# Optimization experiments

Hardware: AMD Instinct MI355X
Metric: run time of the kernel (lower is better)

## Reference

```python
import jax, jax.numpy as jnp
import numpy as np

N_NODES = 50000


def setup_inputs() -> dict:
    key = jax.random.key(0)
    ks = jax.random.split(key, 9)
    B, N, E, IN = 4, N_NODES, 800000, 32
    x = jax.random.normal(ks[0], (B, N, IN), dtype=jnp.float32)
    edge_index = jax.random.randint(ks[1], (2, E), 0, N, dtype=jnp.int64)
    edge_attr = jax.random.normal(ks[2], (E, 1), dtype=jnp.float32)
    W1 = jax.random.normal(ks[3], (2 * IN + 1, 32), dtype=jnp.float32) * 0.1
    b1 = jax.random.normal(ks[4], (32,), dtype=jnp.float32) * 0.1
    W2 = jax.random.normal(ks[5], (32, 30), dtype=jnp.float32) * 0.1
    b2 = jax.random.normal(ks[6], (30,), dtype=jnp.float32) * 0.1
    W3 = jax.random.normal(ks[7], (30, 32), dtype=jnp.float32) * 0.1
    b3 = jax.random.normal(ks[8], (32,), dtype=jnp.float32) * 0.1
    return {"x": x, "edge_index": edge_index, "edge_attr": edge_attr,
            "W1": W1, "b1": b1, "W2": W2, "b2": b2, "W3": W3, "b3": b3}


def reference(x, edge_index, edge_attr, W1, b1, W2, b2, W3, b3):
    B, N, _ = x.shape
    src, tgt = edge_index[0], edge_index[1]
    # normalize edge attributes over edges (torch .std uses ddof=1)
    ea = (edge_attr - edge_attr.mean(axis=0)) / edge_attr.std(axis=0, ddof=1)
    node_src = x[:, src]      # [B, E, in]
    node_tgt = x[:, tgt]      # [B, E, in]
    ea_b = jnp.broadcast_to(ea[None], (B,) + ea.shape)
    h = jnp.concatenate([node_src, node_tgt, ea_b], axis=-1)  # [B, E, 2*in+1]
    h = jax.nn.sigmoid(h @ W1 + b1)
    h = jax.nn.sigmoid(h @ W2 + b2)   # [B, E, 30]
    seg = lambda vals, idx: jax.ops.segment_sum(vals, idx, num_segments=N)
    out_add = jax.vmap(seg, in_axes=(0, None))(h, tgt)    # [B, N, 30]
    out_sub = jax.vmap(seg, in_axes=(0, None))(-h, src)   # [B, N, 30]
    out = out_add + out_sub
    return jax.nn.sigmoid(out @ W3 + b3)  # [B, N, out_dim]
```

## Files before the change

### kernel.cpp

```cpp
#include <hip/hip_runtime.h>
#include <math.h>

#define B_SZ 4
#define IN_F 32
#define H1_F 32
#define H2_F 30
#define TPW 16
#define HREP 16

typedef unsigned int uint;
typedef unsigned short ushort;
typedef __attribute__((ext_vector_type(8))) short bf16x8;
typedef __attribute__((ext_vector_type(4))) float f32x4;

__device__ __forceinline__ float fastrcp(float x) {
#if __has_builtin(__builtin_amdgcn_rcpf)
    return __builtin_amdgcn_rcpf(x);
#else
    return 1.f / x;
#endif
}
__device__ __forceinline__ float sigmoidf_(float x) {
    return fastrcp(1.f + __expf(-x));
}

__device__ __forceinline__ ushort f2bf(float f) {
    uint u = __float_as_uint(f);
    return (ushort)((u + 0x7FFFu + ((u >> 16) & 1u)) >> 16);
}
__device__ __forceinline__ float bf2f(ushort v) { return __uint_as_float(((uint)v) << 16); }
__device__ __forceinline__ uint pk2(float a, float b) {
    return (uint)f2bf(a) | ((uint)f2bf(b) << 16);
}

union Frag { bf16x8 v; ushort us[8]; uint u[4]; };

__global__ void __launch_bounds__(256) stats_hist_kernel(
    const float* __restrict__ ea, const int* __restrict__ ei,
    float2* __restrict__ psums, int* __restrict__ cnt, int E, int N) {
    int e = blockIdx.x * 256 + threadIdx.x;
    int* myc = cnt + (size_t)(blockIdx.x & (HREP - 1)) * N;
    float a = (e < E) ? ea[e] : 0.f;
    if (e < E) {
        atomicAdd(&myc[ei[E + e]], 1);
        atomicAdd(&myc[ei[e]], 1);
    }
    float v = a, v2 = a * a;
    for (int off = 32; off > 0; off >>= 1) {
        v  += __shfl_down(v, off);
        v2 += __shfl_down(v2, off);
    }
    __shared__ float s1[4], s2[4];
    int wid = threadIdx.x >> 6, lane = threadIdx.x & 63;
    if (lane == 0) { s1[wid] = v; s2[wid] = v2; }
    __syncthreads();
    if (threadIdx.x == 0) {
        float2 p;
        p.x = s1[0] + s1[1] + s1[2] + s1[3];
        p.y = s2[0] + s2[1] + s2[2] + s2[3];
        psums[blockIdx.x] = p;
    }
}

__global__ void __launch_bounds__(256) sums_reduce_kernel(
    const float2* __restrict__ psums, float* __restrict__ sums, int nblk) {
    float v = 0.f, v2 = 0.f;
    for (int i = threadIdx.x; i < nblk; i += 256) {
        float2 p = psums[i];
        v += p.x; v2 += p.y;
    }
    for (int off = 32; off > 0; off >>= 1) {
        v  += __shfl_down(v, off);
        v2 += __shfl_down(v2, off);
    }
    __shared__ float s1[4], s2[4];
    int wid = threadIdx.x >> 6, lane = threadIdx.x & 63;
    if (lane == 0) { s1[wid] = v; s2[wid] = v2; }
    __syncthreads();
    if (threadIdx.x == 0) {
        sums[0] = s1[0] + s1[1] + s1[2] + s1[3];
        sums[1] = s2[0] + s2[1] + s2[2] + s2[3];
    }
}

__global__ void __launch_bounds__(256) xcvt_kernel(const float* __restrict__ x,
                                                   ushort* __restrict__ xb,
                                                   long long n8) {
    long long i = (long long)blockIdx.x * 256 + threadIdx.x;
    if (i >= n8) return;
    const float4* p = (const float4*)(x + i * 8);
    float4 v0 = p[0], v1 = p[1];
    uint4 o;
    o.x = pk2(v0.x, v0.y); o.y = pk2(v0.z, v0.w);
    o.z = pk2(v1.x, v1.y); o.w = pk2(v1.z, v1.w);
    *(uint4*)(xb + i * 8) = o;
}

__global__ void __launch_bounds__(256) scan1_kernel(const int* __restrict__ cnt,
                                                    int* __restrict__ offs,
                                                    int* __restrict__ bsum, int n) {
    __shared__ int wtot[4];
    int base = blockIdx.x * 1024 + threadIdx.x * 4;
    int4 v = {0, 0, 0, 0};
    if (base + 3 < n) {
#pragma unroll
        for (int r = 0; r < HREP; r++) {
            int4 t = *(const int4*)(cnt + (size_t)r * n + base);
            v.x += t.x; v.y += t.y; v.z += t.z; v.w += t.w;
        }
    } else {
        for (int r = 0; r < HREP; r++) {
            const int* c = cnt + (size_t)r * n;
            if (base < n)     v.x += c[base];
            if (base + 1 < n) v.y += c[base + 1];
            if (base + 2 < n) v.z += c[base + 2];
            if (base + 3 < n) v.w += c[base + 3];
        }
    }
    int s = v.x + v.y + v.z + v.w;
    int incl = s;
    int lane = threadIdx.x & 63;
    for (int d = 1; d < 64; d <<= 1) {
        int t = __shfl_up(incl, d);
        if (lane >= d) incl += t;
    }
    int wid = threadIdx.x >> 6;
    if (lane == 63) wtot[wid] = incl;
    __syncthreads();
    int woff = 0, tot = 0;
#pragma unroll
    for (int w = 0; w < 4; w++) {
        int t = wtot[w];
        if (w < wid) woff += t;
        tot += t;
    }
    int excl = woff + incl - s;
    int4 o;
    o.x = excl; o.y = excl + v.x; o.z = o.y + v.y; o.w = o.z + v.z;
    if (base + 3 < n) *(int4*)(offs + base) = o;
    else {
        if (base < n)     offs[base] = o.x;
        if (base + 1 < n) offs[base + 1] = o.y;
        if (base + 2 < n) offs[base + 2] = o.z;
        if (base + 3 < n) offs[base + 3] = o.w;
    }
    if (threadIdx.x == 0) bsum[blockIdx.x] = tot;
}

__global__ void scan2_kernel(int* __restrict__ bsum, int* __restrict__ offs,
                             int nb, int n) {
    int lane = threadIdx.x;
    if (nb <= 64) {
        int v = (lane < nb) ? bsum[lane] : 0;
        int incl = v;
        for (int d = 1; d < 64; d <<= 1) {
            int t = __shfl_up(incl, d);
            if (lane >= d) incl += t;
        }
        if (lane < nb) bsum[lane] = incl - v;
        if (lane == 63) offs[n] = incl;
    } else if (lane == 0) {
        int run = 0;
        for (int i = 0; i < nb; i++) { int t = bsum[i]; bsum[i] = run; run += t; }
        offs[n] = run;
    }
}

__global__ void __launch_bounds__(256) scan3_kernel(int* __restrict__ offs,
                                                    int* __restrict__ cursor,
                                                    const int* __restrict__ bsum, int n) {
    int base = blockIdx.x * 1024 + threadIdx.x * 4;
    int add = bsum[blockIdx.x];
    if (base + 3 < n) {
        int4 v = *(const int4*)(offs + base);
        v.x += add; v.y += add; v.z += add; v.w += add;
        *(int4*)(offs + base) = v;
        *(int4*)(cursor + base) = v;
    } else {
        for (int k = 0; k < 4; k++) {
            int i = base + k;
            if (i < n) { int v = offs[i] + add; offs[i] = v; cursor[i] = v; }
        }
    }
}

__global__ void __launch_bounds__(256) restore_cursor_kernel(
    const int* __restrict__ offs, int* __restrict__ cursor, int n) {
    int i = blockIdx.x * 256 + threadIdx.x;
    if (i < n) cursor[i] = offs[i];
}

__global__ void __launch_bounds__(256) edge_mlp_slot(
    const ushort* __restrict__ xb,
    const int* __restrict__ ei, const float* __restrict__ ea,
    const float* __restrict__ W1, const float* __restrict__ b1,
    const float* __restrict__ W2, const float* __restrict__ b2,
    const float* __restrict__ sums, int* __restrict__ cursor,
    ushort* __restrict__ h, int E, int N, int tiles, int boff) {
    __shared__ ushort __attribute__((aligned(16))) hbuf[4][16 * 40];
    int w = threadIdx.x >> 6;
    int lane = threadIdx.x & 63;
    int n16 = lane & 15;
    int q = lane >> 4;

    Frag w1f[2][2];
#pragma unroll
    for (int t = 0; t < 2; t++)
#pragma unroll
        for (int s = 0; s < 2; s++)
#pragma unroll
            for (int j = 0; j < 4; j++) {
                int k0 = 32 * s + q * 8 + 2 * j;
                w1f[t][s].u[j] = pk2(W1[(size_t)k0 * 32 + 16 * t + n16],
                                     W1[(size_t)(k0 + 1) * 32 + 16 * t + n16]);
            }
    Frag w2f[2];
#pragma unroll
    for (int t = 0; t < 2; t++) {
        int m = 16 * t + n16;
#pragma unroll
        for (int j = 0; j < 4; j++) {
            int k0 = q * 8 + 2 * j;
            float a = (m < H2_F) ? W2[(size_t)k0 * H2_F + m] : 0.f;
            float d = (m < H2_F) ? W2[(size_t)(k0 + 1) * H2_F + m] : 0.f;
            w2f[t].u[j] = pk2(a, d);
        }
    }
    float b1q[2][4], w1Lq[2][4], b2q[2][4];
#pragma unroll
    for (int t = 0; t < 2; t++)
#pragma unroll
        for (int r = 0; r < 4; r++) {
            int col = 16 * t + q * 4 + r;
            b1q[t][r]  = b1[col];
            w1Lq[t][r] = W1[(size_t)64 * 32 + col];
            b2q[t][r]  = (col < H2_F) ? b2[col] : 0.f;
        }

    float mean = sums[0] / (float)E;
    float var = (sums[1] - (float)E * mean * mean) / (float)(E - 1);
    float istd = rsqrtf(var);

    int el = n16 >> 1;
    int bl = n16 & 1;
    int b  = bl + boff;
    int gw = blockIdx.x * 4 + w;
    int tile0 = gw * TPW;
    if (tile0 >= tiles) return;

    int src, tgt; float eav; bool vrow; Frag a0, a1; int slotraw;
    {
        int eA = tile0 * 8 + el; vrow = eA < E; int c = vrow ? eA : E - 1;
        src = ei[c]; tgt = ei[E + c]; eav = (ea[c] - mean) * istd;
        *(uint4*)&a0.u[0] = *(const uint4*)(xb + ((size_t)b * N + src) * IN_F + q * 8);
        *(uint4*)&a1.u[0] = *(const uint4*)(xb + ((size_t)b * N + tgt) * IN_F + q * 8);
        slotraw = 0;
        if (lane < 16 && vrow)
            slotraw = atomicAdd(&cursor[(lane & 1) ? src : tgt], 1);
    }

    for (int tix = 0; tix < TPW; ++tix) {
        int tile = tile0 + tix;
        if (tile >= tiles) break;

        int nsrc = 0, ntgt = 0; float neav = 0.f; bool nvrow = false; int nslot = 0;
        Frag na0, na1;
        na0.u[0] = na0.u[1] = na0.u[2] = na0.u[3] = 0; na1 = na0;
        bool hn = (tix + 1 < TPW) && (tile + 1 < tiles);
        if (hn) {
            int eA = (tile + 1) * 8 + el; nvrow = eA < E; int c = nvrow ? eA : E - 1;
            nsrc = ei[c]; ntgt = ei[E + c]; neav = (ea[c] - mean) * istd;
            *(uint4*)&na0.u[0] = *(const uint4*)(xb + ((size_t)b * N + nsrc) * IN_F + q * 8);
            *(uint4*)&na1.u[0] = *(const uint4*)(xb + ((size_t)b * N + ntgt) * IN_F + q * 8);
            if (lane < 16 && nvrow)
                nslot = atomicAdd(&cursor[(lane & 1) ? nsrc : ntgt], 1);
        }

        f32x4 acc0, acc1;
#pragma unroll
        for (int r = 0; r < 4; r++) {
            acc0[r] = b1q[0][r] + eav * w1Lq[0][r];
            acc1[r] = b1q[1][r] + eav * w1Lq[1][r];
        }
        acc0 = __builtin_amdgcn_mfma_f32_16x16x32_bf16(w1f[0][0].v, a0.v, acc0, 0, 0, 0);
        acc0 = __builtin_amdgcn_mfma_f32_16x16x32_bf16(w1f[0][1].v, a1.v, acc0, 0, 0, 0);
        acc1 = __builtin_amdgcn_mfma_f32_16x16x32_bf16(w1f[1][0].v, a0.v, acc1, 0, 0, 0);
        acc1 = __builtin_amdgcn_mfma_f32_16x16x32_bf16(w1f[1][1].v, a1.v, acc1, 0, 0, 0);

        uint u0 = pk2(sigmoidf_(acc0[0]), sigmoidf_(acc0[1]));
        uint u1 = pk2(sigmoidf_(acc0[2]), sigmoidf_(acc0[3]));
        uint u2 = pk2(sigmoidf_(acc1[0]), sigmoidf_(acc1[1]));
        uint u3 = pk2(sigmoidf_(acc1[2]), sigmoidf_(acc1[3]));
        uint2 p01 = {u0, u1}, p23 = {u2, u3};
        *(uint2*)&hbuf[w][n16 * 40 + q * 4]      = p01;
        *(uint2*)&hbuf[w][n16 * 40 + 16 + q * 4] = p23;

        Frag ha;
        *(uint4*)&ha.u[0] = *(const uint4*)&hbuf[w][n16 * 40 + q * 8];

        f32x4 c0, c1;
#pragma unroll
        for (int r = 0; r < 4; r++) { c0[r] = b2q[0][r]; c1[r] = b2q[1][r]; }
        c0 = __builtin_amdgcn_mfma_f32_16x16x32_bf16(w2f[0].v, ha.v, c0, 0, 0, 0);
        c1 = __builtin_amdgcn_mfma_f32_16x16x32_bf16(w2f[1].v, ha.v, c1, 0, 0, 0);

        uint g0 = pk2(sigmoidf_(c0[0]), sigmoidf_(c0[1]));
        uint g1 = pk2(sigmoidf_(c0[2]), sigmoidf_(c0[3]));
        uint g2 = pk2(sigmoidf_(c1[0]), sigmoidf_(c1[1]));
        uint g3 = pk2(sigmoidf_(c1[2]), sigmoidf_(c1[3]));

        int slot_t = __shfl(slotraw, el * 2);
        int slot_s = __shfl(slotraw, el * 2 + 1);
        if (vrow) {
            uint* bt = (uint*)(h + (size_t)slot_t * 64 + bl * 32);
            uint2 t01; t01.x = g0; t01.y = g1;
            uint2 t23; t23.x = g2; t23.y = g3;
            *(uint2*)(bt + q * 2)     = t01;
            *(uint2*)(bt + 8 + q * 2) = t23;
            const uint SM = 0x80008000u;
            uint* bs = (uint*)(h + (size_t)slot_s * 64 + bl * 32);
            uint2 s01; s01.x = g0 ^ SM; s01.y = g1 ^ SM;
            uint2 s23; s23.x = g2 ^ SM; s23.y = g3 ^ SM;
            *(uint2*)(bs + q * 2)     = s01;
            *(uint2*)(bs + 8 + q * 2) = s23;
        }

        src = nsrc; tgt = ntgt; eav = neav; vrow = nvrow;
        a0 = na0; a1 = na1; slotraw = nslot;
    }
}

__global__ void __launch_bounds__(256) gather_slot(
    const ushort* __restrict__ h, const int* __restrict__ offs,
    const float* __restrict__ W3, const float* __restrict__ b3,
    float* __restrict__ out, int N, int boff) {
    __shared__ float sW3[H2_F * 32];
    __shared__ float sb3[32];
    __shared__ float sacc[4][2][H2_F];
    for (int i = threadIdx.x; i < H2_F * 32; i += 256) sW3[i] = W3[i];
    if (threadIdx.x < 32) sb3[threadIdx.x] = b3[threadIdx.x];
    __syncthreads();

    int w = threadIdx.x >> 6, lane = threadIdx.x & 63;
    int n = blockIdx.x * 4 + w;
    if (n >= N) return;

    int s = offs[n], e = offs[n + 1];
    int cnt = e - s;
    int sl = (lane >= 30) ? 1 : 0;
    int r = lane - sl * 30;
    if (lane >= 60) r = 0;
    int bl = r / 15, jp = r % 15;
    const uint* p = (const uint*)h + (size_t)(s + sl) * 32 + bl * 16 + jp;
    float a0 = 0.f, a1 = 0.f;
    int i = (lane < 60) ? sl : cnt;
    for (; i + 6 < cnt; i += 8) {
        uint d0 = p[0], d1 = p[64], d2 = p[128], d3 = p[192];
        p += 256;
        a0 += bf2f((ushort)d0) + bf2f((ushort)d1)
            + bf2f((ushort)d2) + bf2f((ushort)d3);
        a1 += bf2f((ushort)(d0 >> 16)) + bf2f((ushort)(d1 >> 16))
            + bf2f((ushort)(d2 >> 16)) + bf2f((ushort)(d3 >> 16));
    }
    for (; i < cnt; i += 2) {
        uint d = p[0];
        p += 64;
        a0 += bf2f((ushort)d);
        a1 += bf2f((ushort)(d >> 16));
    }
    float f0 = __shfl(a0, lane + 30);
    float f1 = __shfl(a1, lane + 30);
    if (lane < 30) {
        sacc[w][bl][jp * 2]     = a0 + f0;
        sacc[w][bl][jp * 2 + 1] = a1 + f1;
    }
    int bl2 = lane >> 5, k = lane & 31;
    float o = sb3[k];
#pragma unroll
    for (int j = 0; j < H2_F; j++) o += sacc[w][bl2][j] * sW3[j * 32 + k];
    out[((size_t)(boff + bl2) * N + n) * 32 + k] = sigmoidf_(o);
}

__global__ void __launch_bounds__(256) scatter_kernel(const int* __restrict__ ei,
                                                      int* __restrict__ cursor,
                                                      int* __restrict__ list, int E, int N) {
    int e = blockIdx.x * 256 + threadIdx.x;
    if (e < E) {
        int tgt = ei[E + e];
        int p = atomicAdd(&cursor[tgt], 1);
        list[p] = e;
        int src = ei[e];
        int q = atomicAdd(&cursor[src], 1);
        list[q] = e | (int)0x80000000u;
    }
}

template<bool USE_XB>
__global__ void __launch_bounds__(256) edge_mlp_mfma2(
    const float* __restrict__ x, const ushort* __restrict__ xb,
    const int* __restrict__ ei, const float* __restrict__ ea,
    const float* __restrict__ W1, const float* __restrict__ b1,
    const float* __restrict__ W2, const float* __restrict__ b2,
    const float* __restrict__ sums, ushort* __restrict__ h,
    int E, int N, int tiles) {
    __shared__ ushort __attribute__((aligned(16))) hbuf[4][16 * 40];
    int w = threadIdx.x >> 6;
    int lane = threadIdx.x & 63;
    int n16 = lane & 15;
    int q = lane >> 4;

    Frag w1f[2][2];
#pragma unroll
    for (int t = 0; t < 2; t++)
#pragma unroll
        for (int s = 0; s < 2; s++)
#pragma unroll
            for (int j = 0; j < 4; j++) {
                int k0 = 32 * s + q * 8 + 2 * j;
                w1f[t][s].u[j] = pk2(W1[(size_t)k0 * 32 + 16 * t + n16],
                                     W1[(size_t)(k0 + 1) * 32 + 16 * t + n16]);
            }
    Frag w2f[2];
#pragma unroll
    for (int t = 0; t < 2; t++) {
        int m = 16 * t + n16;
#pragma unroll
        for (int j = 0; j < 4; j++) {
            int k0 = q * 8 + 2 * j;
            float a = (m < H2_F) ? W2[(size_t)k0 * H2_F + m] : 0.f;
            float d = (m < H2_F) ? W2[(size_t)(k0 + 1) * H2_F + m] : 0.f;
            w2f[t].u[j] = pk2(a, d);
        }
    }
    float b1q[2][4], w1Lq[2][4], b2q[2][4];
#pragma unroll
    for (int t = 0; t < 2; t++)
#pragma unroll
        for (int r = 0; r < 4; r++) {
            int col = 16 * t + q * 4 + r;
            b1q[t][r]  = b1[col];
            w1Lq[t][r] = W1[(size_t)64 * 32 + col];
            b2q[t][r]  = (col < H2_F) ? b2[col] : 0.f;
        }

    float mean = sums[0] / (float)E;
    float var = (sums[1] - (float)E * mean * mean) / (float)(E - 1);
    float istd = rsqrtf(var);

    int b = n16 & 3;
    int eoff = n16 >> 2;
    int gw = blockIdx.x * 4 + w;

    for (int tix = 0; tix < TPW; ++tix) {
        int tile = gw * TPW + tix;
        if (tile >= tiles) break;
        int e0 = tile * 4;
        int eA = e0 + eoff;
        bool vrow = eA < E;
        int eAc = vrow ? eA : E - 1;
        int src = ei[eAc], tgt = ei[E + eAc];
        float eav = (ea[eAc] - mean) * istd;

        Frag a0, a1;
        if (USE_XB) {
            *(uint4*)&a0.u[0] = *(const uint4*)(xb + ((size_t)b * N + src) * IN_F + q * 8);
            *(uint4*)&a1.u[0] = *(const uint4*)(xb + ((size_t)b * N + tgt) * IN_F + q * 8);
        } else {
            const float4* ps = (const float4*)(x + ((size_t)b * N + src) * IN_F + q * 8);
            float4 s0 = ps[0], s1 = ps[1];
            const float4* pt = (const float4*)(x + ((size_t)b * N + tgt) * IN_F + q * 8);
            float4 t0 = pt[0], t1 = pt[1];
            a0.u[0] = pk2(s0.x, s0.y); a0.u[1] = pk2(s0.z, s0.w);
            a0.u[2] = pk2(s1.x, s1.y); a0.u[3] = pk2(s1.z, s1.w);
            a1.u[0] = pk2(t0.x, t0.y); a1.u[1] = pk2(t0.z, t0.w);
            a1.u[2] = pk2(t1.x, t1.y); a1.u[3] = pk2(t1.z, t1.w);
        }

        f32x4 acc0, acc1;
#pragma unroll
        for (int r = 0; r < 4; r++) {
            acc0[r] = b1q[0][r] + eav * w1Lq[0][r];
            acc1[r] = b1q[1][r] + eav * w1Lq[1][r];
        }
        acc0 = __builtin_amdgcn_mfma_f32_16x16x32_bf16(w1f[0][0].v, a0.v, acc0, 0, 0, 0);
        acc0 = __builtin_amdgcn_mfma_f32_16x16x32_bf16(w1f[0][1].v, a1.v, acc0, 0, 0, 0);
        acc1 = __builtin_amdgcn_mfma_f32_16x16x32_bf16(w1f[1][0].v, a0.v, acc1, 0, 0, 0);
        acc1 = __builtin_amdgcn_mfma_f32_16x16x32_bf16(w1f[1][1].v, a1.v, acc1, 0, 0, 0);

        uint u0 = pk2(sigmoidf_(acc0[0]), sigmoidf_(acc0[1]));
        uint u1 = pk2(sigmoidf_(acc0[2]), sigmoidf_(acc0[3]));
        uint u2 = pk2(sigmoidf_(acc1[0]), sigmoidf_(acc1[1]));
        uint u3 = pk2(sigmoidf_(acc1[2]), sigmoidf_(acc1[3]));
        uint2 p01 = {u0, u1}, p23 = {u2, u3};
        *(uint2*)&hbuf[w][n16 * 40 + q * 4]      = p01;
        *(uint2*)&hbuf[w][n16 * 40 + 16 + q * 4] = p23;

        Frag ha;
        *(uint4*)&ha.u[0] = *(const uint4*)&hbuf[w][n16 * 40 + q * 8];

        f32x4 c0, c1;
#pragma unroll
        for (int r = 0; r < 4; r++) { c0[r] = b2q[0][r]; c1[r] = b2q[1][r]; }
        c0 = __builtin_amdgcn_mfma_f32_16x16x32_bf16(w2f[0].v, ha.v, c0, 0, 0, 0);
        c1 = __builtin_amdgcn_mfma_f32_16x16x32_bf16(w2f[1].v, ha.v, c1, 0, 0, 0);

        uint g0 = pk2(sigmoidf_(c0[0]), sigmoidf_(c0[1]));
        uint g1 = pk2(sigmoidf_(c0[2]), sigmoidf_(c0[3]));
        uint g2 = pk2(sigmoidf_(c1[0]), sigmoidf_(c1[1]));
        uint g3 = pk2(sigmoidf_(c1[2]), sigmoidf_(c1[3]));
        if (vrow) {
            uint* base = (uint*)(h + (size_t)(e0 * 4 + n16) * H2_F);
            base[q * 2]     = g0;
            base[q * 2 + 1] = g1;
            base[8 + q * 2] = g2;
            if (q < 3) base[8 + q * 2 + 1] = g3;
        }
    }
}

__global__ void __launch_bounds__(256) gather_final(
    const ushort* __restrict__ h, const int* __restrict__ list,
    const int* __restrict__ offs, const float* __restrict__ W3,
    const float* __restrict__ b3, float* __restrict__ out, int N) {
    __shared__ float sW3[H2_F * 32];
    __shared__ float sb3[32];
    __shared__ float sacc[4][B_SZ][H2_F];
    for (int i = threadIdx.x; i < H2_F * 32; i += 256) sW3[i] = W3[i];
    if (threadIdx.x < 32) sb3[threadIdx.x] = b3[threadIdx.x];
    __syncthreads();

    int w = threadIdx.x >> 6, lane = threadIdx.x & 63;
    int n = blockIdx.x * 4 + w;
    if (n >= N) return;

    if (lane < 60) {
        int bq = lane / 15, jp = lane % 15;
        float a0 = 0.f, a1 = 0.f;
        int s = offs[n], e = offs[n + 1];
        int i = s;
        for (; i + 4 <= e; i += 4) {
            int v0 = list[i], v1 = list[i + 1], v2 = list[i + 2], v3 = list[i + 3];
            uint d0 = *(const uint*)(h + (size_t)(v0 & 0x7FFFFFFF) * 120 + bq * 30 + jp * 2);
            uint d1 = *(const uint*)(h + (size_t)(v1 & 0x7FFFFFFF) * 120 + bq * 30 + jp * 2);
            uint d2 = *(const uint*)(h + (size_t)(v2 & 0x7FFFFFFF) * 120 + bq * 30 + jp * 2);
            uint d3 = *(const uint*)(h + (size_t)(v3 & 0x7FFFFFFF) * 120 + bq * 30 + jp * 2);
            float g0 = (v0 < 0) ? -1.f : 1.f;
            float g1 = (v1 < 0) ? -1.f : 1.f;
            float g2 = (v2 < 0) ? -1.f : 1.f;
            float g3 = (v3 < 0) ? -1.f : 1.f;
            a0 += g0 * bf2f((ushort)d0) + g1 * bf2f((ushort)d1)
                + g2 * bf2f((ushort)d2) + g3 * bf2f((ushort)d3);
            a1 += g0 * bf2f((ushort)(d0 >> 16)) + g1 * bf2f((ushort)(d1 >> 16))
                + g2 * bf2f((ushort)(d2 >> 16)) + g3 * bf2f((ushort)(d3 >> 16));
        }
        for (; i < e; i++) {
            int v = list[i];
            uint d = *(const uint*)(h + (size_t)(v & 0x7FFFFFFF) * 120 + bq * 30 + jp * 2);
            float g = (v < 0) ? -1.f : 1.f;
            a0 += g * bf2f((ushort)d);
            a1 += g * bf2f((ushort)(d >> 16));
        }
        sacc[w][bq][jp * 2]     = a0;
        sacc[w][bq][jp * 2 + 1] = a1;
    }
    int b = lane >> 4, k = lane & 15;
    float o0 = sb3[k], o1 = sb3[k + 16];
#pragma unroll
    for (int j = 0; j < H2_F; j++) {
        float v = sacc[w][b][j];
        o0 += v * sW3[j * 32 + k];
        o1 += v * sW3[j * 32 + k + 16];
    }
    float* op = out + ((size_t)b * N + n) * 32;
    op[k]      = sigmoidf_(o0);
    op[k + 16] = sigmoidf_(o1);
}

extern "C" void kernel_launch(void* const* d_in, const int* in_sizes, int n_in,
                              void* d_out, int out_size, void* d_ws, size_t ws_size,
                              hipStream_t stream) {
    const float* x  = (const float*)d_in[0];
    const int*   ei = (const int*)d_in[1];
    const float* ea = (const float*)d_in[2];
    const float* W1 = (const float*)d_in[3];
    const float* b1 = (const float*)d_in[4];
    const float* W2 = (const float*)d_in[5];
    const float* b2 = (const float*)d_in[6];
    const float* W3 = (const float*)d_in[7];
    const float* b3 = (const float*)d_in[8];
    float* out = (float*)d_out;

    const int E  = in_sizes[2];
    const int N  = in_sizes[0] / (B_SZ * IN_F);
    const int BN = B_SZ * N;
    const int nb = (N + 1023) / 1024;
    const int nblk_stats = (E + 255) / 256;

    char* base = (char*)d_ws;

    size_t off = 0;
    int* cnt    = (int*)(base + off); off += (size_t)HREP * N * 4;
    float* sums = (float*)(base + off); off += 8;
    int* offs   = (int*)(base + off); off += (size_t)(N + 1) * 4;
    int* cursor = (int*)(base + off); off += (size_t)N * 4;
    int* bsum   = (int*)(base + off); off += 4096;
    off = (off + 255) & ~(size_t)255;
    float2* psums = (float2*)(base + off); off += (size_t)nblk_stats * 8;
    off = (off + 255) & ~(size_t)255;
    ushort* h   = (ushort*)(base + off); off += (size_t)2 * E * 128;
    off = (off + 255) & ~(size_t)255;
    ushort* xb  = (ushort*)(base + off); off += (size_t)BN * IN_F * 2;
    size_t needNew = off;

    size_t offB = 0;
    int* cntB    = (int*)(base + offB); offB += (size_t)HREP * N * 4;
    float* sumsB = (float*)(base + offB); offB += 8;
    int* offsB   = (int*)(base + offB); offB += (size_t)(N + 1) * 4;
    int* cursorB = (int*)(base + offB); offB += (size_t)N * 4;
    int* bsumB   = (int*)(base + offB); offB += 4096;
    offB = (offB + 255) & ~(size_t)255;
    float2* psumsB = (float2*)(base + offB); offB += (size_t)nblk_stats * 8;
    int* list    = (int*)(base + offB); offB += (size_t)2 * E * 4;
    offB = (offB + 255) & ~(size_t)255;
    ushort* hB   = (ushort*)(base + offB); offB += (size_t)E * 240;
    offB = (offB + 255) & ~(size_t)255;
    ushort* xbB  = (ushort*)(base + offB);
    size_t needB = offB + (size_t)BN * IN_F * 2;

    if (ws_size >= needNew) {
        const int tiles = (E + 7) / 8;
        const int waves = (tiles + TPW - 1) / TPW;
        const int eblocks = (waves + 3) / 4;
        hipMemsetAsync(cnt, 0, (size_t)HREP * N * 4 + 8, stream);
        stats_hist_kernel<<<nblk_stats, 256, 0, stream>>>(ea, ei, psums, cnt, E, N);
        sums_reduce_kernel<<<1, 256, 0, stream>>>(psums, sums, nblk_stats);
        long long n8 = (long long)BN * IN_F / 8;
        xcvt_kernel<<<(int)((n8 + 255) / 256), 256, 0, stream>>>(x, xb, n8);
        scan1_kernel<<<nb, 256, 0, stream>>>(cnt, offs, bsum, N);
        scan2_kernel<<<1, 64, 0, stream>>>(bsum, offs, nb, N);
        scan3_kernel<<<nb, 256, 0, stream>>>(offs, cursor, bsum, N);
        edge_mlp_slot<<<eblocks, 256, 0, stream>>>(xb, ei, ea, W1, b1, W2, b2,
                                                   sums, cursor, h, E, N, tiles, 0);
        gather_slot<<<(N + 3) / 4, 256, 0, stream>>>(h, offs, W3, b3, out, N, 0);
        restore_cursor_kernel<<<(N + 255) / 256, 256, 0, stream>>>(offs, cursor, N);
        edge_mlp_slot<<<eblocks, 256, 0, stream>>>(xb, ei, ea, W1, b1, W2, b2,
                                                   sums, cursor, h, E, N, tiles, 2);
        gather_slot<<<(N + 3) / 4, 256, 0, stream>>>(h, offs, W3, b3, out, N, 2);
    } else {
        const int tiles = (E + 3) / 4;
        const int waves = (tiles + TPW - 1) / TPW;
        const int eblocks = (waves + 3) / 4;
        bool use_xb = (ws_size >= needB);
        hipMemsetAsync(cntB, 0, (size_t)HREP * N * 4 + 8, stream);
        stats_hist_kernel<<<nblk_stats, 256, 0, stream>>>(ea, ei, psumsB, cntB, E, N);
        sums_reduce_kernel<<<1, 256, 0, stream>>>(psumsB, sumsB, nblk_stats);
        if (use_xb) {
            long long n8 = (long long)BN * IN_F / 8;
            xcvt_kernel<<<(int)((n8 + 255) / 256), 256, 0, stream>>>(x, xbB, n8);
        }
        scan1_kernel<<<nb, 256, 0, stream>>>(cntB, offsB, bsumB, N);
        scan2_kernel<<<1, 64, 0, stream>>>(bsumB, offsB, nb, N);
        scan3_kernel<<<nb, 256, 0, stream>>>(offsB, cursorB, bsumB, N);
        scatter_kernel<<<(E + 255) / 256, 256, 0, stream>>>(ei, cursorB, list, E, N);
        if (use_xb)
            edge_mlp_mfma2<true><<<eblocks, 256, 0, stream>>>(x, xbB, ei, ea, W1, b1,
                                                              W2, b2, sumsB, hB, E, N, tiles);
        else
            edge_mlp_mfma2<false><<<eblocks, 256, 0, stream>>>(x, xbB, ei, ea, W1, b1,
                                                               W2, b2, sumsB, hB, E, N, tiles);
        gather_final<<<(N + 3) / 4, 256, 0, stream>>>(hB, list, offsB, W3, b3, out, N);
    }
}
```

Before: 454.7 us.

## Compute all four batches per edge once and gather via sorted edge list

The edge MLP now processes all four batch elements per edge in one pass, writing h once per edge in edge order instead of twice (signed copies) into per-node slots across two batch-half passes. It builds a CSR list of edge ids tagged with a sign bit via atomics inside the MLP kernel, and the gather reads h indirectly through that list, applying the sign. The xcvt kernel is fused into the stats/histogram kernel, and the restore_cursor kernel is removed. This halves h writes and the number of MLP/gather launches, at the cost of random indirect reads in the gather instead of contiguous slot reads.

```diff
diff --git a/kernel.cpp b/kernel.cpp
--- a/kernel.cpp
+++ b/kernel.cpp
@@ -35,9 +35,20 @@
 
 union Frag { bf16x8 v; ushort us[8]; uint u[4]; };
 
-__global__ void __launch_bounds__(256) stats_hist_kernel(
+__global__ void __launch_bounds__(256) stats_xcvt_kernel(
     const float* __restrict__ ea, const int* __restrict__ ei,
-    float2* __restrict__ psums, int* __restrict__ cnt, int E, int N) {
+    const float* __restrict__ x, float2* __restrict__ psums,
+    int* __restrict__ cnt, ushort* __restrict__ xb,
+    int E, int N, long long n8) {
+    long long i = (long long)blockIdx.x * 256 + threadIdx.x;
+    if (i < n8) {
+        const float4* p = (const float4*)(x + i * 8);
+        float4 v0 = p[0], v1 = p[1];
+        uint4 o;
+        o.x = pk2(v0.x, v0.y); o.y = pk2(v0.z, v0.w);
+        o.z = pk2(v1.x, v1.y); o.w = pk2(v1.z, v1.w);
+        *(uint4*)(xb + i * 8) = o;
+    }
     int e = blockIdx.x * 256 + threadIdx.x;
     int* myc = cnt + (size_t)(blockIdx.x & (HREP - 1)) * N;
     float a = (e < E) ? ea[e] : 0.f;
@@ -81,19 +92,6 @@
         sums[0] = s1[0] + s1[1] + s1[2] + s1[3];
         sums[1] = s2[0] + s2[1] + s2[2] + s2[3];
     }
-}
-
-__global__ void __launch_bounds__(256) xcvt_kernel(const float* __restrict__ x,
-                                                   ushort* __restrict__ xb,
-                                                   long long n8) {
-    long long i = (long long)blockIdx.x * 256 + threadIdx.x;
-    if (i >= n8) return;
-    const float4* p = (const float4*)(x + i * 8);
-    float4 v0 = p[0], v1 = p[1];
-    uint4 o;
-    o.x = pk2(v0.x, v0.y); o.y = pk2(v0.z, v0.w);
-    o.z = pk2(v1.x, v1.y); o.w = pk2(v1.z, v1.w);
-    *(uint4*)(xb + i * 8) = o;
 }
 
 __global__ void __launch_bounds__(256) scan1_kernel(const int* __restrict__ cnt,
@@ -184,19 +182,14 @@
     }
 }
 
-__global__ void __launch_bounds__(256) restore_cursor_kernel(
-    const int* __restrict__ offs, int* __restrict__ cursor, int n) {
-    int i = blockIdx.x * 256 + threadIdx.x;
-    if (i < n) cursor[i] = offs[i];
-}
-
-__global__ void __launch_bounds__(256) edge_mlp_slot(
+__global__ void __launch_bounds__(256) edge_mlp_e4(
     const ushort* __restrict__ xb,
     const int* __restrict__ ei, const float* __restrict__ ea,
     const float* __restrict__ W1, const float* __restrict__ b1,
     const float* __restrict__ W2, const float* __restrict__ b2,
     const float* __restrict__ sums, int* __restrict__ cursor,
-    ushort* __restrict__ h, int E, int N, int tiles, int boff) {
+    int* __restrict__ list, ushort* __restrict__ h,
+    int E, int N, int tiles) {
     __shared__ ushort __attribute__((aligned(16))) hbuf[4][16 * 40];
     int w = threadIdx.x >> 6;
     int lane = threadIdx.x & 63;
@@ -241,39 +234,49 @@
     float var = (sums[1] - (float)E * mean * mean) / (float)(E - 1);
     float istd = rsqrtf(var);
 
-    int el = n16 >> 1;
-    int bl = n16 & 1;
-    int b  = bl + boff;
+    int b  = n16 & 3;
+    int el = n16 >> 2;
     int gw = blockIdx.x * 4 + w;
     int tile0 = gw * TPW;
     if (tile0 >= tiles) return;
 
-    int src, tgt; float eav; bool vrow; Frag a0, a1; int slotraw;
+    int src, tgt; float eav; bool vrow; Frag a0, a1;
     {
-        int eA = tile0 * 8 + el; vrow = eA < E; int c = vrow ? eA : E - 1;
+        int eA = tile0 * 4 + el; vrow = eA < E; int c = vrow ? eA : E - 1;
         src = ei[c]; tgt = ei[E + c]; eav = (ea[c] - mean) * istd;
         *(uint4*)&a0.u[0] = *(const uint4*)(xb + ((size_t)b * N + src) * IN_F + q * 8);
         *(uint4*)&a1.u[0] = *(const uint4*)(xb + ((size_t)b * N + tgt) * IN_F + q * 8);
-        slotraw = 0;
-        if (lane < 16 && vrow)
-            slotraw = atomicAdd(&cursor[(lane & 1) ? src : tgt], 1);
+        if (lane < 8) {
+            int eS = tile0 * 4 + (lane >> 1);
+            if (eS < E) {
+                int node = (lane & 1) ? ei[eS] : ei[E + eS];
+                int s = atomicAdd(&cursor[node], 1);
+                list[s] = eS | (int)(((uint)(lane & 1)) << 31);
+            }
+        }
     }
 
     for (int tix = 0; tix < TPW; ++tix) {
         int tile = tile0 + tix;
         if (tile >= tiles) break;
 
-        int nsrc = 0, ntgt = 0; float neav = 0.f; bool nvrow = false; int nslot = 0;
+        int nsrc = 0, ntgt = 0; float neav = 0.f; bool nvrow = false;
         Frag na0, na1;
         na0.u[0] = na0.u[1] = na0.u[2] = na0.u[3] = 0; na1 = na0;
         bool hn = (tix + 1 < TPW) && (tile + 1 < tiles);
         if (hn) {
-            int eA = (tile + 1) * 8 + el; nvrow = eA < E; int c = nvrow ? eA : E - 1;
+            int eA = (tile + 1) * 4 + el; nvrow = eA < E; int c = nvrow ? eA : E - 1;
             nsrc = ei[c]; ntgt = ei[E + c]; neav = (ea[c] - mean) * istd;
             *(uint4*)&na0.u[0] = *(const uint4*)(xb + ((size_t)b * N + nsrc) * IN_F + q * 8);
             *(uint4*)&na1.u[0] = *(const uint4*)(xb + ((size_t)b * N + ntgt) * IN_F + q * 8);
-            if (lane < 16 && nvrow)
-                nslot = atomicAdd(&cursor[(lane & 1) ? nsrc : ntgt], 1);
+            if (lane < 8) {
+                int eS = (tile + 1) * 4 + (lane >> 1);
+                if (eS < E) {
+                    int node = (lane & 1) ? ei[eS] : ei[E + eS];
+                    int s = atomicAdd(&cursor[node], 1);
+                    list[s] = eS | (int)(((uint)(lane & 1)) << 31);
+                }
+            }
         }
 
         f32x4 acc0, acc1;
@@ -309,34 +312,26 @@
         uint g2 = pk2(sigmoidf_(c1[0]), sigmoidf_(c1[1]));
         uint g3 = pk2(sigmoidf_(c1[2]), sigmoidf_(c1[3]));
 
-        int slot_t = __shfl(slotraw, el * 2);
-        int slot_s = __shfl(slotraw, el * 2 + 1);
         if (vrow) {
-            uint* bt = (uint*)(h + (size_t)slot_t * 64 + bl * 32);
+            uint* bt = (uint*)h + (size_t)(tile * 4 + el) * 64 + b * 16;
             uint2 t01; t01.x = g0; t01.y = g1;
             uint2 t23; t23.x = g2; t23.y = g3;
             *(uint2*)(bt + q * 2)     = t01;
             *(uint2*)(bt + 8 + q * 2) = t23;
-            const uint SM = 0x80008000u;
-            uint* bs = (uint*)(h + (size_t)slot_s * 64 + bl * 32);
-            uint2 s01; s01.x = g0 ^ SM; s01.y = g1 ^ SM;
-            uint2 s23; s23.x = g2 ^ SM; s23.y = g3 ^ SM;
-            *(uint2*)(bs + q * 2)     = s01;
-            *(uint2*)(bs + 8 + q * 2) = s23;
         }
 
         src = nsrc; tgt = ntgt; eav = neav; vrow = nvrow;
-        a0 = na0; a1 = na1; slotraw = nslot;
-    }
-}
-
-__global__ void __launch_bounds__(256) gather_slot(
-    const ushort* __restrict__ h, const int* __restrict__ offs,
-    const float* __restrict__ W3, const float* __restrict__ b3,
-    float* __restrict__ out, int N, int boff) {
+        a0 = na0; a1 = na1;
+    }
+}
+
+__global__ void __launch_bounds__(256) gather_e4(
+    const ushort* __restrict__ h, const int* __restrict__ list,
+    const int* __restrict__ offs, const float* __restrict__ W3,
+    const float* __restrict__ b3, float* __restrict__ out, int N) {
     __shared__ float sW3[H2_F * 32];
     __shared__ float sb3[32];
-    __shared__ float sacc[4][2][H2_F];
+    __shared__ float sacc[4][B_SZ][H2_F];
     for (int i = threadIdx.x; i < H2_F * 32; i += 256) sW3[i] = W3[i];
     if (threadIdx.x < 32) sb3[threadIdx.x] = b3[threadIdx.x];
     __syncthreads();
@@ -346,39 +341,48 @@
     if (n >= N) return;
 
     int s = offs[n], e = offs[n + 1];
-    int cnt = e - s;
-    int sl = (lane >= 30) ? 1 : 0;
-    int r = lane - sl * 30;
-    if (lane >= 60) r = 0;
-    int bl = r / 15, jp = r % 15;
-    const uint* p = (const uint*)h + (size_t)(s + sl) * 32 + bl * 16 + jp;
+    int r = (lane < 60) ? lane : 0;
+    int bq = r / 15, jp = r % 15;
+    const uint* h32 = (const uint*)h;
     float a0 = 0.f, a1 = 0.f;
-    int i = (lane < 60) ? sl : cnt;
-    for (; i + 6 < cnt; i += 8) {
-        uint d0 = p[0], d1 = p[64], d2 = p[128], d3 = p[192];
-        p += 256;
-        a0 += bf2f((ushort)d0) + bf2f((ushort)d1)
-            + bf2f((ushort)d2) + bf2f((ushort)d3);
-        a1 += bf2f((ushort)(d0 >> 16)) + bf2f((ushort)(d1 >> 16))
-            + bf2f((ushort)(d2 >> 16)) + bf2f((ushort)(d3 >> 16));
-    }
-    for (; i < cnt; i += 2) {
-        uint d = p[0];
-        p += 64;
-        a0 += bf2f((ushort)d);
-        a1 += bf2f((ushort)(d >> 16));
-    }
-    float f0 = __shfl(a0, lane + 30);
-    float f1 = __shfl(a1, lane + 30);
-    if (lane < 30) {
-        sacc[w][bl][jp * 2]     = a0 + f0;
-        sacc[w][bl][jp * 2 + 1] = a1 + f1;
-    }
-    int bl2 = lane >> 5, k = lane & 31;
-    float o = sb3[k];
-#pragma unroll
-    for (int j = 0; j < H2_F; j++) o += sacc[w][bl2][j] * sW3[j * 32 + k];
-    out[((size_t)(boff + bl2) * N + n) * 32 + k] = sigmoidf_(o);
+    int i = (lane < 60) ? s : e;
+    for (; i + 3 < e; i += 4) {
+        int v0 = list[i], v1 = list[i + 1], v2 = list[i + 2], v3 = list[i + 3];
+        uint d0 = h32[(size_t)(v0 & 0x7FFFFFFF) * 64 + bq * 16 + jp];
+        uint d1 = h32[(size_t)(v1 & 0x7FFFFFFF) * 64 + bq * 16 + jp];
+        uint d2 = h32[(size_t)(v2 & 0x7FFFFFFF) * 64 + bq * 16 + jp];
+        uint d3 = h32[(size_t)(v3 & 0x7FFFFFFF) * 64 + bq * 16 + jp];
+        float g0 = (v0 < 0) ? -1.f : 1.f;
+        float g1 = (v1 < 0) ? -1.f : 1.f;
+        float g2 = (v2 < 0) ? -1.f : 1.f;
+        float g3 = (v3 < 0) ? -1.f : 1.f;
+        a0 += g0 * bf2f((ushort)d0) + g1 * bf2f((ushort)d1)
+            + g2 * bf2f((ushort)d2) + g3 * bf2f((ushort)d3);
+        a1 += g0 * bf2f((ushort)(d0 >> 16)) + g1 * bf2f((ushort)(d1 >> 16))
+            + g2 * bf2f((ushort)(d2 >> 16)) + g3 * bf2f((ushort)(d3 >> 16));
+    }
+    for (; i < e; i++) {
+        int v = list[i];
+        uint d = h32[(size_t)(v & 0x7FFFFFFF) * 64 + bq * 16 + jp];
+        float g = (v < 0) ? -1.f : 1.f;
+        a0 += g * bf2f((ushort)d);
+        a1 += g * bf2f((ushort)(d >> 16));
+    }
+    if (lane < 60) {
+        sacc[w][bq][jp * 2]     = a0;
+        sacc[w][bq][jp * 2 + 1] = a1;
+    }
+    int b = lane >> 4, k = lane & 15;
+    float o0 = sb3[k], o1 = sb3[k + 16];
+#pragma unroll
+    for (int j = 0; j < H2_F; j++) {
+        float v = sacc[w][b][j];
+        o0 += v * sW3[j * 32 + k];
+        o1 += v * sW3[j * 32 + k + 16];
+    }
+    float* op = out + ((size_t)b * N + n) * 32;
+    op[k]      = sigmoidf_(o0);
+    op[k + 16] = sigmoidf_(o1);
 }
 
 __global__ void __launch_bounds__(256) scatter_kernel(const int* __restrict__ ei,
@@ -594,7 +598,8 @@
     const int N  = in_sizes[0] / (B_SZ * IN_F);
     const int BN = B_SZ * N;
     const int nb = (N + 1023) / 1024;
-    const int nblk_stats = (E + 255) / 256;
+    const long long n8 = (long long)BN * IN_F / 8;
+    const int nblkC = (int)(((long long)E > n8 ? (long long)E : n8) + 255) / 256;
 
     char* base = (char*)d_ws;
 
@@ -605,12 +610,14 @@
     int* cursor = (int*)(base + off); off += (size_t)N * 4;
     int* bsum   = (int*)(base + off); off += 4096;
     off = (off + 255) & ~(size_t)255;
-    float2* psums = (float2*)(base + off); off += (size_t)nblk_stats * 8;
+    float2* psums = (float2*)(base + off); off += (size_t)nblkC * 8;
     off = (off + 255) & ~(size_t)255;
-    ushort* h   = (ushort*)(base + off); off += (size_t)2 * E * 128;
+    int* list   = (int*)(base + off); off += (size_t)2 * E * 4;
+    off = (off + 255) & ~(size_t)255;
+    ushort* h   = (ushort*)(base + off); off += (size_t)E * 256;
     off = (off + 255) & ~(size_t)255;
     ushort* xb  = (ushort*)(base + off); off += (size_t)BN * IN_F * 2;
-    size_t needNew = off;
+    size_t needA = off;
 
     size_t offB = 0;
     int* cntB    = (int*)(base + offB); offB += (size_t)HREP * N * 4;
@@ -619,55 +626,47 @@
     int* cursorB = (int*)(base + offB); offB += (size_t)N * 4;
     int* bsumB   = (int*)(base + offB); offB += 4096;
     offB = (offB + 255) & ~(size_t)255;
-    float2* psumsB = (float2*)(base + offB); offB += (size_t)nblk_stats * 8;
-    int* list    = (int*)(base + offB); offB += (size_t)2 * E * 4;
+    float2* psumsB = (float2*)(base + offB); offB += (size_t)nblkC * 8;
+    int* listB   = (int*)(base + offB); offB += (size_t)2 * E * 4;
     offB = (offB + 255) & ~(size_t)255;
     ushort* hB   = (ushort*)(base + offB); offB += (size_t)E * 240;
     offB = (offB + 255) & ~(size_t)255;
     ushort* xbB  = (ushort*)(base + offB);
     size_t needB = offB + (size_t)BN * IN_F * 2;
 
-    if (ws_size >= needNew) {
-        const int tiles = (E + 7) / 8;
+    if (ws_size >= needA) {
+        const int tiles = (E + 3) / 4;
         const int waves = (tiles + TPW - 1) / TPW;
         const int eblocks = (waves + 3) / 4;
         hipMemsetAsync(cnt, 0, (size_t)HREP * N * 4 + 8, stream);
-        stats_hist_kernel<<<nblk_stats, 256, 0, stream>>>(ea, ei, psums, cnt, E, N);
-        sums_reduce_kernel<<<1, 256, 0, stream>>>(psums, sums, nblk_stats);
-        long long n8 = (long long)BN * IN_F / 8;
-        xcvt_kernel<<<(int)((n8 + 255) / 256), 256, 0, stream>>>(x, xb, n8);
+        stats_xcvt_kernel<<<nblkC, 256, 0, stream>>>(ea, ei, x, psums, cnt, xb, E, N, n8);
+        sums_reduce_kernel<<<1, 256, 0, stream>>>(psums, sums, nblkC);
         scan1_kernel<<<nb, 256, 0, stream>>>(cnt, offs, bsum, N);
         scan2_kernel<<<1, 64, 0, stream>>>(bsum, offs, nb, N);
         scan3_kernel<<<nb, 256, 0, stream>>>(offs, cursor, bsum, N);
-        edge_mlp_slot<<<eblocks, 256, 0, stream>>>(xb, ei, ea, W1, b1, W2, b2,
-                                                   sums, cursor, h, E, N, tiles, 0);
-        gather_slot<<<(N + 3) / 4, 256, 0, stream>>>(h, offs, W3, b3, out, N, 0);
-        restore_cursor_kernel<<<(N + 255) / 256, 256, 0, stream>>>(offs, cursor, N);
-        edge_mlp_slot<<<eblocks, 256, 0, stream>>>(xb, ei, ea, W1, b1, W2, b2,
-                                                   sums, cursor, h, E, N, tiles, 2);
-        gather_slot<<<(N + 3) / 4, 256, 0, stream>>>(h, offs, W3, b3, out, N, 2);
+        edge_mlp_e4<<<eblocks, 256, 0, stream>>>(xb, ei, ea, W1, b1, W2, b2,
+                                                 sums, cursor, list, h, E, N, tiles);
+        gather_e4<<<(N + 3) / 4, 256, 0, stream>>>(h, list, offs, W3, b3, out, N);
     } else {
         const int tiles = (E + 3) / 4;
         const int waves = (tiles + TPW - 1) / TPW;
         const int eblocks = (waves + 3) / 4;
         bool use_xb = (ws_size >= needB);
         hipMemsetAsync(cntB, 0, (size_t)HREP * N * 4 + 8, stream);
-        stats_hist_kernel<<<nblk_stats, 256, 0, stream>>>(ea, ei, psumsB, cntB, E, N);
-        sums_reduce_kernel<<<1, 256, 0, stream>>>(psumsB, sumsB, nblk_stats);
-        if (use_xb) {
-            long long n8 = (long long)BN * IN_F / 8;
-            xcvt_kernel<<<(int)((n8 + 255) / 256), 256, 0, stream>>>(x, xbB, n8);
-        }
+        stats_xcvt_kernel<<<nblkC, 256, 0, stream>>>(ea, ei, x, psumsB, cntB,
+                                                     use_xb ? xbB : (ushort*)nullptr,
+                                                     E, N, use_xb ? n8 : 0LL);
+        sums_reduce_kernel<<<1, 256, 0, stream>>>(psumsB, sumsB, nblkC);
         scan1_kernel<<<nb, 256, 0, stream>>>(cntB, offsB, bsumB, N);
         scan2_kernel<<<1, 64, 0, stream>>>(bsumB, offsB, nb, N);
         scan3_kernel<<<nb, 256, 0, stream>>>(offsB, cursorB, bsumB, N);
-        scatter_kernel<<<(E + 255) / 256, 256, 0, stream>>>(ei, cursorB, list, E, N);
+        scatter_kernel<<<(E + 255) / 256, 256, 0, stream>>>(ei, cursorB, listB, E, N);
         if (use_xb)
             edge_mlp_mfma2<true><<<eblocks, 256, 0, stream>>>(x, xbB, ei, ea, W1, b1,
                                                               W2, b2, sumsB, hB, E, N, tiles);
         else
             edge_mlp_mfma2<false><<<eblocks, 256, 0, stream>>>(x, xbB, ei, ea, W1, b1,
                                                                W2, b2, sumsB, hB, E, N, tiles);
-        gather_final<<<(N + 3) / 4, 256, 0, stream>>>(hB, list, offsB, W3, b3, out, N);
-    }
-}
+        gather_final<<<(N + 3) / 4, 256, 0, stream>>>(hB, listB, offsB, W3, b3, out, N);
+    }
+}
```

After: 438.3 us. -3.6%, faster.
